# Performance work log

Hardware: AMD Instinct MI355X
Metric: run time of the kernel (lower is better)

The kernel has to match this reference:

```python
import jax, jax.numpy as jnp
import numpy as np

B, N, T, W, H, ED, S, C, E = 16, 256, 64, 12, 64, 64, 5, 4, 2048
ALPHA = 1.0
FG = W + H  # gcn_in_channels = window_size + tgcn_hidden_dim


def setup_inputs() -> dict:
    key = jax.random.key(0)
    ks = jax.random.split(key, 26)
    rn = lambda k, shape: jax.random.normal(k, shape, jnp.float32) * 0.1
    x = jax.random.normal(ks[0], (B, N, T), jnp.float32)
    src = jax.random.randint(ks[1], (E,), 0, N)
    off = jax.random.randint(ks[2], (E,), 1, N)
    dst = (src + off) % N  # no self loops
    return {
        'x': x,
        'static_edge_weight': jax.random.uniform(ks[3], (E,), jnp.float32),
        'gsl_gconv_w': rn(ks[4], (FG, ED)), 'gsl_gconv_b': rn(ks[5], (ED,)),
        'gsl_w1': rn(ks[6], (ED, ED)), 'gsl_b1': rn(ks[7], (ED,)),
        'gsl_w2': rn(ks[8], (ED, ED)), 'gsl_b2': rn(ks[9], (ED,)),
        'wz_c': rn(ks[10], (1, H)), 'bz_c': rn(ks[11], (H,)),
        'wz_l': rn(ks[12], (2 * H, H)), 'bz_l': rn(ks[13], (H,)),
        'wr_c': rn(ks[14], (1, H)), 'br_c': rn(ks[15], (H,)),
        'wr_l': rn(ks[16], (2 * H, H)), 'br_l': rn(ks[17], (H,)),
        'wh_c': rn(ks[18], (1, H)), 'bh_c': rn(ks[19], (H,)),
        'wh_l': rn(ks[20], (2 * H, H)), 'bh_l': rn(ks[21], (H,)),
        'cls_w': rn(ks[22], (N * H, C)), 'cls_b': rn(ks[23], (C,)),
        'static_edge_index': jnp.stack([src, dst]).astype(jnp.int32),
    }


def _normalize(A):
    # GCN sym-norm with added self loops; A has zero diagonal by construction.
    Ahat = A + jnp.eye(N, dtype=A.dtype)
    deg = Ahat.sum(axis=-2)  # in-degree (PyG gcn_norm scatters weight on col)
    dinv = jnp.where(deg > 0, 1.0 / jnp.sqrt(deg), 0.0)
    return dinv[..., :, None] * Ahat * dinv[..., None, :]


def reference(x, static_edge_weight, gsl_gconv_w, gsl_gconv_b, gsl_w1, gsl_b1,
              gsl_w2, gsl_b2, wz_c, bz_c, wz_l, bz_l, wr_c, br_c, wr_l, br_l,
              wh_c, bh_c, wh_l, bh_l, cls_w, cls_b, static_edge_index):
    A_stat = jnp.zeros((N, N), jnp.float32).at[static_edge_index[0], static_edge_index[1]].add(static_edge_weight)
    An_stat = _normalize(A_stat)  # [N,N]

    # Sliding windows, left-padded with zeros to window_size W.
    xp = jnp.pad(x, ((0, 0), (0, 0), (W - 1, 0)))
    widx = jnp.arange(T)[:, None] + jnp.arange(W)[None, :]
    wins = jnp.transpose(xp[:, :, widx], (2, 0, 1, 3))      # [T,B,N,W]
    xts = jnp.transpose(x, (2, 0, 1))[..., None]            # [T,B,N,1]
    cnts = jnp.minimum(jnp.arange(T) + 1, S).astype(jnp.float32)
    idxs = jnp.arange(T) % S

    def gcn_s(X, Wm, b):  # static graph, out[j] = sum_i Anorm[i,j] (XW)[i]
        return jnp.einsum('ij,bif->bjf', An_stat, X @ Wm) + b

    def gcn_d(An, X, Wm, b):  # per-batch dynamic graph
        return jnp.einsum('bij,bif->bjf', An, X @ Wm) + b

    def step(carry, xs):
        h, Eh = carry
        win, xt, cnt, idx = xs
        It = jnp.concatenate([win, h], axis=-1)             # [B,N,W+H]
        df = gcn_s(It, gsl_gconv_w, gsl_gconv_b)
        de1 = jnp.tanh(ALPHA * (df @ gsl_w1 + gsl_b1))
        de2 = jnp.tanh(ALPHA * (df @ gsl_w2 + gsl_b2))
        M12 = jnp.einsum('bie,bje->bij', de1, de2)          # de1 @ de2^T
        Et = jax.nn.relu(jnp.tanh(ALPHA * (M12 - jnp.swapaxes(M12, -1, -2))))
        Eh = Eh.at[:, idx].set(Et)                          # ring buffer write
        Mt = Eh.sum(axis=1) / cnt                           # mean over filled slots
        An = _normalize(Mt)
        cz = gcn_d(An, xt, wz_c, bz_c)
        z = jax.nn.sigmoid(jnp.concatenate([cz, h], -1) @ wz_l + bz_l)
        cr = gcn_d(An, xt, wr_c, br_c)
        r = jax.nn.sigmoid(jnp.concatenate([cr, h], -1) @ wr_l + br_l)
        ch = gcn_d(An, xt, wh_c, bh_c)
        ht = jnp.tanh(jnp.concatenate([ch, h * r], -1) @ wh_l + bh_l)
        h = z * h + (1.0 - z) * ht
        return (h, Eh), None

    h0 = jnp.zeros((B, N, H), jnp.float32)
    Eh0 = jnp.zeros((B, S, N, N), jnp.float32)
    (hT, _), _ = jax.lax.scan(step, (h0, Eh0), (wins, xts, cnts, idxs))
    return hT.reshape(B, N * H) @ cls_w + cls_b
```

## Files before the change

### kernel.cpp

```cpp
#include <hip/hip_runtime.h>
#include <hip/hip_bf16.h>


typedef unsigned short u16;
typedef unsigned int u32;
typedef unsigned long long u64;
typedef __attribute__((ext_vector_type(8))) short bf16x8;
typedef __attribute__((ext_vector_type(4))) float f32x4;

#define B_ 16
#define N_ 256
#define T_ 64
#define W_ 12
#define S_ 5
#define E_ 2048
#define G_ 16

__device__ __forceinline__ float b2f(u16 u) {
  union { u32 i; float f; } v; v.i = ((u32)u) << 16; return v.f;
}
__device__ __forceinline__ u16 f2b(float f) {
  union { float f; u32 i; } v; v.f = f;
  u32 x = v.i; x += 0x7fff + ((x >> 16) & 1); return (u16)(x >> 16);
}
__device__ __forceinline__ float ftanh(float x) {
  float e = __expf(-2.f * fabsf(x));
  float t = (1.f - e) / (1.f + e);
  return x < 0.f ? -t : t;
}
__device__ __forceinline__ float fsigm(float x) { return 1.f / (1.f + __expf(-x)); }
__device__ __forceinline__ float cvload(const void* p, size_t i, int f) {
  return f ? ((const float*)p)[i] : b2f(((const u16*)p)[i]);
}
__device__ __forceinline__ u16 cvloadb(const void* p, size_t i, int f) {
  return f ? f2b(((const float*)p)[i]) : ((const u16*)p)[i];
}
__device__ __forceinline__ float gld(const float* p) {
  return __hip_atomic_load(p, __ATOMIC_RELAXED, __HIP_MEMORY_SCOPE_SYSTEM);
}
__device__ __forceinline__ void gst(float* p, float v) {
  __hip_atomic_store(p, v, __ATOMIC_RELAXED, __HIP_MEMORY_SCOPE_SYSTEM);
}
__device__ __forceinline__ u64 gld64(const u64* p) {
  return __hip_atomic_load(p, __ATOMIC_RELAXED, __HIP_MEMORY_SCOPE_SYSTEM);
}
__device__ __forceinline__ void gst64(u64* p, u64 v) {
  __hip_atomic_store(p, v, __ATOMIC_RELAXED, __HIP_MEMORY_SCOPE_SYSTEM);
}
__device__ __forceinline__ u32 gldu(const u32* p) {
  return __hip_atomic_load(p, __ATOMIC_RELAXED, __HIP_MEMORY_SCOPE_SYSTEM);
}
__device__ __forceinline__ f32x4 mfma16(bf16x8 a, bf16x8 b, f32x4 c) {
  return __builtin_amdgcn_mfma_f32_16x16x32_bf16(a, b, c, 0, 0, 0);
}
__device__ __forceinline__ bf16x8 ldfrag(const u16* p) { return *(const bf16x8*)p; }

struct Params {
  const void *x0, *ew0, *gw0, *gb0, *w10, *b10, *w20, *b20;
  const void *wzc0, *bzc0, *wzl0, *bzl0, *wrc0, *brc0, *wrl0, *brl0;
  const void *whc0, *bhc0, *whl0, *bhl0, *clsw0, *clsb0;
  const int* eidx;
  float *degsum, *Eh, *clspart;
  u64 *de1g, *de2g, *xTp, *hgpT;
  u32 *tags;
  void* out;
};

__device__ __forceinline__ void wtag(const u32* tg, u32 target) {
  const int k = threadIdx.x & 15;
  while (!__all((int)(gldu(&tg[k]) >= target)))
    __builtin_amdgcn_s_sleep(1);
}
__device__ __forceinline__ void wtag8(const u32* tg, int base, u32 target) {
  const int k = base + (threadIdx.x & 7);
  while (!__all((int)(gldu(&tg[k]) >= target)))
    __builtin_amdgcn_s_sleep(1);
}
__device__ __forceinline__ void ptag(u32* tg, int wg, u32 val) {
  if (threadIdx.x == 0)
    __hip_atomic_store(&tg[wg], val, __ATOMIC_RELAXED, __HIP_MEMORY_SCOPE_SYSTEM);
}

__global__ void __launch_bounds__(256, 1) dtgcn_main(Params p) {
  __shared__ __align__(16) u16 s_union[21120];
  __shared__ __align__(16) u16 s_gwF[64 * 104];
  __shared__ __align__(16) u16 s_w1T[64 * 72], s_w2T[64 * 72];
  __shared__ __align__(16) u16 s_gzT[64 * 72], s_grT[64 * 72], s_ghT[64 * 72];
  __shared__ __align__(16) u16 s_antO1[16 * 264], s_antO2[16 * 264];
  __shared__ __align__(16) u16 s_m1[16 * 104];
  __shared__ float s_msum[16 * 257];
  __shared__ __align__(16) u16 s_de1I[16 * 72], s_de2I[16 * 72];
  __shared__ __align__(16) u16 s_hbf[16 * 72];
  __shared__ __align__(16) u16 s_dfhr[16 * 72];
  __shared__ float s_colv[16], s_degacc[16];
  __shared__ float s_y[256], s_dinv[256], s_s[16];
  __shared__ float s_uv[384], s_gb[64], s_b1[64], s_b2[64];
  __shared__ int s_flag;

  const int b = blockIdx.x & 15;
  const int wg = blockIdx.x >> 4;
  const int tid = threadIdx.x;
  const int lane = tid & 63;
  const int wv = tid >> 6;
  const int l = lane & 15;
  const int quad = lane >> 4;
  const int r0 = wg * 16;

  u64* de1g = p.de1g + (size_t)b * N_ * 16;
  u64* de2g = p.de2g + (size_t)b * N_ * 16;
  u64* hgpb = p.hgpT + (size_t)b * 64 * 64;
  u64* xTw  = p.xTp + (size_t)b * 64 * 64;
  const u64* xTb = xTw;
  float* degb = p.degsum + (size_t)b * N_;
  u32* tgDe = p.tags + b * 128;
  u32* tgDg = p.tags + b * 128 + 16;
  u32* tgH  = p.tags + b * 128 + 32;
  u32* tgX  = p.tags + b * 128 + 48;
  u32* tgC  = p.tags + b * 128 + 64;

  if (tid == 0) {
    const u16* q = (const u16*)p.x0;
    int c = 0;
    for (int i = 0; i < 256; ++i) {
      int ex = (q[i] >> 7) & 0xff;
      c += (ex >= 110 && ex <= 135);
    }
    s_flag = (c < 200) ? 1 : 0;
  }
  __syncthreads();
  const int fl = s_flag;

  {
    u16* xs = s_union;
    #pragma unroll
    for (int r = 0; r < 4; ++r) {
      const int tt = wg * 4 + r;
      xs[r * 256 + tid] = f2b(cvload(p.x0, ((size_t)b * N_ + tid) * T_ + tt, fl));
    }
    __syncthreads();
    const int r = tid >> 6, c = tid & 63;
    u64 v = (u64)xs[r * 256 + 4 * c]
          | ((u64)xs[r * 256 + 4 * c + 1] << 16)
          | ((u64)xs[r * 256 + 4 * c + 2] << 32)
          | ((u64)xs[r * 256 + 4 * c + 3] << 48);
    gst64(&xTw[(size_t)(wg * 4 + r) * 64 + c], v);
    __syncthreads();
    ptag(tgX, wg, 1);
  }

  {
    float* s_acol = (float*)s_union;
    float* s_dg   = (float*)s_union + 4096;
    for (int i = tid; i < 4096; i += 256) s_acol[i] = 0.f;
    s_dg[tid] = 0.f;
    __syncthreads();
    for (int e2 = tid; e2 < E_; e2 += 256) {
      const int sN = p.eidx[e2], dN = p.eidx[E_ + e2];
      const float wv2 = cvload(p.ew0, e2, fl);
      atomicAdd(&s_dg[dN], wv2);
      const int dl = dN - r0;
      if (dl >= 0 && dl < 16) atomicAdd(&s_acol[sN * 16 + dl], wv2);
    }
    __syncthreads();
    s_dg[tid] = rsqrtf(1.f + s_dg[tid]);
    __syncthreads();
    for (int idx = tid; idx < 4096; idx += 256) {
      const int jl = idx >> 8, i = idx & 255;
      float a = s_acol[i * 16 + jl] + ((i == r0 + jl) ? 1.f : 0.f);
      float v = s_dg[i] * a * s_dg[r0 + jl];
      u16 hi = f2b(v);
      s_antO1[jl * 264 + i] = hi;
      s_antO2[jl * 264 + i] = f2b(v - b2f(hi));
    }
  }

  for (int idx = tid; idx < 64 * 104; idx += 256) {
    const int ee = idx / 104, k = idx - ee * 104;
    u16 v = 0;
    if (k < 64) v = cvloadb(p.gw0, (12 + k) * 64 + ee, fl);
    else if (k < 76) v = cvloadb(p.gw0, (k - 64) * 64 + ee, fl);
    s_gwF[ee * 104 + k] = v;
  }
  for (int idx = tid; idx < 4096; idx += 256) {
    const int ee = idx >> 6, ff = idx & 63;
    s_w1T[ee * 72 + ff] = cvloadb(p.w10, ff * 64 + ee, fl);
    s_w2T[ee * 72 + ff] = cvloadb(p.w20, ff * 64 + ee, fl);
    s_gzT[ee * 72 + ff] = cvloadb(p.wzl0, 4096 + ff * 64 + ee, fl);
    s_grT[ee * 72 + ff] = cvloadb(p.wrl0, 4096 + ff * 64 + ee, fl);
    s_ghT[ee * 72 + ff] = cvloadb(p.whl0, 4096 + ff * 64 + ee, fl);
  }
  if (tid < 64) {
    const int e2 = tid;
    float uz = 0, vz = 0, ur = 0, vr = 0, uh = 0, vh = 0;
    for (int f = 0; f < 64; ++f) {
      float wz = cvload(p.wzl0, f * 64 + e2, fl);
      float wr = cvload(p.wrl0, f * 64 + e2, fl);
      float wh = cvload(p.whl0, f * 64 + e2, fl);
      uz += cvload(p.wzc0, f, fl) * wz; vz += cvload(p.bzc0, f, fl) * wz;
      ur += cvload(p.wrc0, f, fl) * wr; vr += cvload(p.brc0, f, fl) * wr;
      uh += cvload(p.whc0, f, fl) * wh; vh += cvload(p.bhc0, f, fl) * wh;
    }
    s_uv[0 * 64 + e2] = uz; s_uv[1 * 64 + e2] = vz + cvload(p.bzl0, e2, fl);
    s_uv[2 * 64 + e2] = ur; s_uv[3 * 64 + e2] = vr + cvload(p.brl0, e2, fl);
    s_uv[4 * 64 + e2] = uh; s_uv[5 * 64 + e2] = vh + cvload(p.bhl0, e2, fl);
    s_gb[tid] = cvload(p.gb0, tid, fl);
    s_b1[tid] = cvload(p.b10, tid, fl);
    s_b2[tid] = cvload(p.b20, tid, fl);
  }
  for (int idx = tid; idx < 16 * 257; idx += 256) s_msum[idx] = 0.f;
  for (int idx = tid; idx < 16 * 72; idx += 256) s_hbf[idx] = 0;
  for (int idx = tid; idx < 16 * 104; idx += 256) s_m1[idx] = 0;
  for (int idx = 20064 + tid; idx < 21120; idx += 256) s_union[idx] = 0;
  if (tid < 16) s_degacc[tid] = 0.f;
  __syncthreads();

  u16* s_itT = s_union;
  u16* s_j1  = s_union;
  u16* s_j2  = s_union + 9216;

  float hreg[4] = {0.f, 0.f, 0.f, 0.f};
  const int e = wv * 16 + l;

  for (int t = 0; t < T_; ++t) {
    float xv;
    {
      if (t == 0) wtag(tgX, 1);
      xv = cvload(p.x0, ((size_t)b * N_ + tid) * T_ + t, fl);
      u64 tw0[2], tw1[2];
      #pragma unroll
      for (int q = 0; q < 2; ++q) {
        const int idx = q * 256 + tid;
        const int row = idx >> 5, c = idx & 31;
        const bool ok = idx < 384;
        const int tx = t - (W_ - 1) + row;
        const bool live = ok && tx >= 0;
        tw0[q] = live ? gld64(&xTb[(size_t)tx * 64 + c]) : 0ull;
        tw1[q] = live ? gld64(&xTb[(size_t)tx * 64 + 32 + c]) : 0ull;
      }
      wtag8(tgH, 0, (u32)t);
      {
        u64 th[8];
        #pragma unroll
        for (int q = 0; q < 8; ++q) {
          const int idx = q * 256 + tid;
          const int row = idx >> 5, c = idx & 31;
          th[q] = gld64(&hgpb[(size_t)row * 64 + c]);
        }
        #pragma unroll
        for (int q = 0; q < 8; ++q) {
          const int idx = q * 256 + tid;
          const int row = idx >> 5, c = idx & 31;
          *(u64*)&s_itT[row * 264 + c * 4] = th[q];
        }
        #pragma unroll
        for (int q = 0; q < 2; ++q) {
          const int idx = q * 256 + tid;
          if (idx < 384) {
            const int row = idx >> 5, c = idx & 31;
            *(u64*)&s_itT[(64 + row) * 264 + c * 4] = tw0[q];
          }
        }
      }
      __syncthreads();
      wtag8(tgH, 8, (u32)t);
      u64 th1[8];
      #pragma unroll
      for (int q = 0; q < 8; ++q) {
        const int idx = q * 256 + tid;
        const int row = idx >> 5, c = idx & 31;
        th1[q] = gld64(&hgpb[(size_t)row * 64 + 32 + c]);
      }
      f32x4 accA[2];
      accA[0] = (f32x4){0.f, 0.f, 0.f, 0.f};
      accA[1] = (f32x4){0.f, 0.f, 0.f, 0.f};
      {
        int ti = 0;
        for (int nt = wv; nt < 5; nt += 4, ++ti) {
          #pragma unroll
          for (int ch = 0; ch < 4; ++ch) {
            const int io = ch * 32 + quad * 8;
            bf16x8 bfr = ldfrag(&s_itT[(nt * 16 + l) * 264 + io]);
            accA[ti] = mfma16(ldfrag(&s_antO1[l * 264 + io]), bfr, accA[ti]);
            accA[ti] = mfma16(ldfrag(&s_antO2[l * 264 + io]), bfr, accA[ti]);
          }
        }
      }
      #pragma unroll
      for (int q = 0; q < 8; ++q) {
        const int idx = q * 256 + tid;
        const int row = idx >> 5, c = idx & 31;
        *(u64*)&s_itT[row * 264 + (32 + c) * 4] = th1[q];
      }
      #pragma unroll
      for (int q = 0; q < 2; ++q) {
        const int idx = q * 256 + tid;
        if (idx < 384) {
          const int row = idx >> 5, c = idx & 31;
          *(u64*)&s_itT[(64 + row) * 264 + (32 + c) * 4] = tw1[q];
        }
      }
      __syncthreads();
      {
        int ti = 0;
        for (int nt = wv; nt < 5; nt += 4, ++ti) {
          #pragma unroll
          for (int ch = 4; ch < 8; ++ch) {
            const int io = ch * 32 + quad * 8;
            bf16x8 bfr = ldfrag(&s_itT[(nt * 16 + l) * 264 + io]);
            accA[ti] = mfma16(ldfrag(&s_antO1[l * 264 + io]), bfr, accA[ti]);
            accA[ti] = mfma16(ldfrag(&s_antO2[l * 264 + io]), bfr, accA[ti]);
          }
          #pragma unroll
          for (int r = 0; r < 4; ++r)
            s_m1[(quad * 4 + r) * 104 + nt * 16 + l] = f2b(accA[ti][r]);
        }
      }
      __syncthreads();
      {
        f32x4 dfa = {0.f, 0.f, 0.f, 0.f};
        #pragma unroll
        for (int ks = 0; ks < 3; ++ks) {
          bf16x8 afr = ldfrag(&s_m1[l * 104 + ks * 32 + quad * 8]);
          dfa = mfma16(afr, ldfrag(&s_gwF[e * 104 + ks * 32 + quad * 8]), dfa);
        }
        #pragma unroll
        for (int r = 0; r < 4; ++r)
          s_dfhr[(quad * 4 + r) * 72 + e] = f2b(dfa[r] + s_gb[e]);
      }
      __syncthreads();
      {
        f32x4 E1, E2;
        #pragma unroll
        for (int r = 0; r < 4; ++r) { E1[r] = s_b1[e]; E2[r] = s_b2[e]; }
        #pragma unroll
        for (int ks = 0; ks < 2; ++ks) {
          bf16x8 afr = ldfrag(&s_dfhr[l * 72 + ks * 32 + quad * 8]);
          E1 = mfma16(afr, ldfrag(&s_w1T[e * 72 + ks * 32 + quad * 8]), E1);
          E2 = mfma16(afr, ldfrag(&s_w2T[e * 72 + ks * 32 + quad * 8]), E2);
        }
        #pragma unroll
        for (int r = 0; r < 4; ++r) {
          s_de1I[(quad * 4 + r) * 72 + e] = f2b(ftanh(E1[r]));
          s_de2I[(quad * 4 + r) * 72 + e] = f2b(ftanh(E2[r]));
        }
      }
      __syncthreads();
      {
        const int row = tid >> 4, c = tid & 15;
        u64 v1 = *(const u64*)&s_de1I[row * 72 + c * 4];
        u64 v2 = *(const u64*)&s_de2I[row * 72 + c * 4];
        gst64(&de1g[(size_t)(r0 + row) * 16 + c], v1);
        gst64(&de2g[(size_t)(r0 + row) * 16 + c], v2);
      }
      __syncthreads();
      ptag(tgDe, wg, (u32)(t + 1));
    }

    {
      const int sidx = t % S_;
      float* Ehc = p.Eh + ((size_t)((b * S_ + sidx) * G_ + wg)) * (N_ * 16);
      if (tid < 16) s_colv[tid] = 0.f;
      bf16x8 bq1[2], bq2[2];
      #pragma unroll
      for (int ks = 0; ks < 2; ++ks) {
        bq1[ks] = ldfrag(&s_de1I[l * 72 + ks * 32 + quad * 8]);
        bq2[ks] = ldfrag(&s_de2I[l * 72 + ks * 32 + quad * 8]);
      }
      float old0[2][4], old1[2][4];
      #pragma unroll
      for (int mt2 = 0; mt2 < 2; ++mt2) {
        const int mt = wv * 2 + mt2;
        #pragma unroll
        for (int r = 0; r < 4; ++r) {
          const int i0 = mt * 16 + quad * 4 + r;
          old0[mt2][r] = Ehc[(size_t)i0 * 16 + l];
          old1[mt2][r] = Ehc[(size_t)(128 + i0) * 16 + l];
        }
      }
      wtag8(tgDe, 0, (u32)(t + 1));
      u64 t1a[8], t2a[8];
      #pragma unroll
      for (int q = 0; q < 8; ++q) {
        const int idx = q * 256 + tid;
        const int row = idx >> 4, c = idx & 15;
        t1a[q] = gld64(&de1g[(size_t)row * 16 + c]);
        t2a[q] = gld64(&de2g[(size_t)row * 16 + c]);
      }
      #pragma unroll
      for (int q = 0; q < 8; ++q) {
        const int idx = q * 256 + tid;
        const int row = idx >> 4, c = idx & 15;
        *(u64*)&s_j1[row * 72 + c * 4] = t1a[q];
        *(u64*)&s_j2[row * 72 + c * 4] = t2a[q];
      }
      __syncthreads();
      wtag8(tgDe, 8, (u32)(t + 1));
      u64 t1b[8], t2b[8];
      #pragma unroll
      for (int q = 0; q < 8; ++q) {
        const int idx = q * 256 + tid;
        const int row = idx >> 4, c = idx & 15;
        t1b[q] = gld64(&de1g[(size_t)(128 + row) * 16 + c]);
        t2b[q] = gld64(&de2g[(size_t)(128 + row) * 16 + c]);
      }
      float dcacc = 0.f;
      #pragma unroll
      for (int mt2 = 0; mt2 < 2; ++mt2) {
        const int mt = wv * 2 + mt2;
        f32x4 D1 = {0.f, 0.f, 0.f, 0.f}, D2 = {0.f, 0.f, 0.f, 0.f};
        #pragma unroll
        for (int ks = 0; ks < 2; ++ks) {
          bf16x8 a1 = ldfrag(&s_j1[(mt * 16 + l) * 72 + ks * 32 + quad * 8]);
          bf16x8 a2 = ldfrag(&s_j2[(mt * 16 + l) * 72 + ks * 32 + quad * 8]);
          D1 = mfma16(a1, bq2[ks], D1);
          D2 = mfma16(a2, bq1[ks], D2);
        }
        #pragma unroll
        for (int r = 0; r < 4; ++r) {
          const int i = mt * 16 + quad * 4 + r;
          float d = ftanh(D1[r] - D2[r]);
          float eN = fmaxf(d, 0.f);
          float dd = eN - old0[mt2][r];
          Ehc[(size_t)i * 16 + l] = eN;
          s_msum[l * 257 + i] += dd;
          dcacc += dd;
        }
      }
      __syncthreads();
      #pragma unroll
      for (int q = 0; q < 8; ++q) {
        const int idx = q * 256 + tid;
        const int row = idx >> 4, c = idx & 15;
        *(u64*)&s_j1[row * 72 + c * 4] = t1b[q];
        *(u64*)&s_j2[row * 72 + c * 4] = t2b[q];
      }
      __syncthreads();
      #pragma unroll
      for (int mt2 = 0; mt2 < 2; ++mt2) {
        const int mt = wv * 2 + mt2;
        f32x4 D1 = {0.f, 0.f, 0.f, 0.f}, D2 = {0.f, 0.f, 0.f, 0.f};
        #pragma unroll
        for (int ks = 0; ks < 2; ++ks) {
          bf16x8 a1 = ldfrag(&s_j1[(mt * 16 + l) * 72 + ks * 32 + quad * 8]);
          bf16x8 a2 = ldfrag(&s_j2[(mt * 16 + l) * 72 + ks * 32 + quad * 8]);
          D1 = mfma16(a1, bq2[ks], D1);
          D2 = mfma16(a2, bq1[ks], D2);
        }
        #pragma unroll
        for (int r = 0; r < 4; ++r) {
          const int i = 128 + mt * 16 + quad * 4 + r;
          float d = ftanh(D1[r] - D2[r]);
          float eN = fmaxf(d, 0.f);
          float dd = eN - old1[mt2][r];
          Ehc[(size_t)i * 16 + l] = eN;
          s_msum[l * 257 + i] += dd;
          dcacc += dd;
        }
      }
      dcacc += __shfl_xor(dcacc, 16);
      dcacc += __shfl_xor(dcacc, 32);
      if (lane < 16) atomicAdd(&s_colv[lane], dcacc);
      __syncthreads();
      if (tid < 16) {
        float nd = s_degacc[tid] + s_colv[tid];
        s_degacc[tid] = nd;
        gst(&degb[r0 + tid], nd);
      }
      __syncthreads();
      ptag(tgDg, wg, (u32)(t + 1));
    }

    {
      f32x4 azh = {0.f, 0.f, 0.f, 0.f}, arh = {0.f, 0.f, 0.f, 0.f};
      #pragma unroll
      for (int ks = 0; ks < 2; ++ks) {
        bf16x8 afr = ldfrag(&s_hbf[l * 72 + ks * 32 + quad * 8]);
        azh = mfma16(afr, ldfrag(&s_gzT[e * 72 + ks * 32 + quad * 8]), azh);
        arh = mfma16(afr, ldfrag(&s_grT[e * 72 + ks * 32 + quad * 8]), arh);
      }
      wtag(tgDg, (u32)(t + 1));
      const float cnt = (float)((t + 1 < S_) ? (t + 1) : S_);
      const float invc = 1.f / cnt;
      {
        float dg = 1.f + gld(&degb[tid]) * invc;
        float di = rsqrtf(dg);
        s_dinv[tid] = di;
        s_y[tid] = di * xv;
      }
      __syncthreads();
      {
        const int jl = tid >> 4, cc = tid & 15;
        float part = 0.f;
        #pragma unroll
        for (int k = 0; k < 16; ++k) {
          const int i = cc * 16 + ((k + cc) & 15);
          part += s_msum[jl * 257 + i] * s_y[i];
        }
        part += __shfl_xor(part, 1);
        part += __shfl_xor(part, 2);
        part += __shfl_xor(part, 4);
        part += __shfl_xor(part, 8);
        if (cc == 0) {
          const int j = r0 + jl;
          s_s[jl] = s_dinv[j] * (part * invc + s_y[j]);
        }
      }
      __syncthreads();
      float sv[4];
      #pragma unroll
      for (int r = 0; r < 4; ++r) sv[r] = s_s[quad * 4 + r];
      float zz[4], rr2[4];
      #pragma unroll
      for (int r = 0; r < 4; ++r) {
        zz[r]  = fsigm(azh[r] + s_uv[0 * 64 + e] * sv[r] + s_uv[1 * 64 + e]);
        rr2[r] = fsigm(arh[r] + s_uv[2 * 64 + e] * sv[r] + s_uv[3 * 64 + e]);
      }
      #pragma unroll
      for (int r = 0; r < 4; ++r)
        s_dfhr[(quad * 4 + r) * 72 + e] = f2b(hreg[r] * rr2[r]);
      __syncthreads();
      f32x4 ah;
      #pragma unroll
      for (int r = 0; r < 4; ++r) ah[r] = s_uv[4 * 64 + e] * sv[r] + s_uv[5 * 64 + e];
      #pragma unroll
      for (int ks = 0; ks < 2; ++ks) {
        bf16x8 afr = ldfrag(&s_dfhr[l * 72 + ks * 32 + quad * 8]);
        ah = mfma16(afr, ldfrag(&s_ghT[e * 72 + ks * 32 + quad * 8]), ah);
      }
      #pragma unroll
      for (int r = 0; r < 4; ++r) {
        float ht = ftanh(ah[r]);
        hreg[r] = zz[r] * hreg[r] + (1.f - zz[r]) * ht;
      }
      {
        u16 h0 = f2b(hreg[0]), h1 = f2b(hreg[1]);
        u16 h2 = f2b(hreg[2]), h3 = f2b(hreg[3]);
        u64 hv = (u64)h0 | ((u64)h1 << 16) | ((u64)h2 << 32) | ((u64)h3 << 48);
        gst64(&hgpb[(size_t)e * 64 + (r0 >> 2) + quad], hv);
        s_hbf[(quad * 4 + 0) * 72 + e] = h0;
        s_hbf[(quad * 4 + 1) * 72 + e] = h1;
        s_hbf[(quad * 4 + 2) * 72 + e] = h2;
        s_hbf[(quad * 4 + 3) * 72 + e] = h3;
      }
      __syncthreads();
      ptag(tgH, wg, (u32)(t + 1));
    }
  }

  {
    float part[4] = {0.f, 0.f, 0.f, 0.f};
    #pragma unroll
    for (int r = 0; r < 4; ++r) {
      const size_t base = ((size_t)(r0 + quad * 4 + r) * 64 + e) * 4;
      #pragma unroll
      for (int c = 0; c < 4; ++c)
        part[c] += hreg[r] * cvload(p.clsw0, base + c, fl);
    }
    #pragma unroll
    for (int c = 0; c < 4; ++c) {
      float v = part[c];
      v += __shfl_xor(v, 1);  v += __shfl_xor(v, 2);
      v += __shfl_xor(v, 4);  v += __shfl_xor(v, 8);
      v += __shfl_xor(v, 16); v += __shfl_xor(v, 32);
      if (lane == 0) s_s[wv * 4 + c] = v;
    }
    __syncthreads();
    if (tid < 4) {
      float tot = s_s[0 + tid] + s_s[4 + tid] + s_s[8 + tid] + s_s[12 + tid];
      gst(&p.clspart[(b * 16 + wg) * 4 + tid], tot);
    }
    __syncthreads();
    ptag(tgC, wg, 1);
    if (wg == 0) {
      wtag(tgC, 1);
      if (tid < 4) {
        float v = 0.f;
        for (int k = 0; k < 16; ++k) v += gld(&p.clspart[(b * 16 + k) * 4 + tid]);
        v += cvload(p.clsb0, tid, fl);
        if (fl) ((float*)p.out)[b * 4 + tid] = v;
        else    ((u16*)p.out)[b * 4 + tid] = f2b(v);
      }
    }
  }
}

extern "C" void kernel_launch(void* const* d_in, const int* in_sizes, int n_in,
                              void* d_out, int out_size, void* d_ws, size_t ws_size,
                              hipStream_t stream) {
  float* w = (float*)d_ws;
  size_t o = 0;
  auto alloc = [&](size_t n) { float* r = w + o; o += (n + 63) & ~(size_t)63; return r; };
  u64* de1g = (u64*)alloc((size_t)B_ * N_ * 32);
  u64* de2g = (u64*)alloc((size_t)B_ * N_ * 32);
  u64* xTp  = (u64*)alloc((size_t)B_ * 64 * 128);
  float* clspart = alloc(B_ * 16 * 4);
  const size_t zero_off = o;
  u64*   hgpT  = (u64*)alloc((size_t)B_ * 64 * 128);
  float* degs  = alloc((size_t)B_ * N_);
  u32*   tags  = (u32*)alloc(B_ * 128);
  float* Eh    = alloc((size_t)B_ * S_ * N_ * N_);
  if (ws_size < o * sizeof(float)) return;

  (void)hipMemsetAsync(w + zero_off, 0, (o - zero_off) * sizeof(float), stream);

  Params p;
  p.x0  = d_in[0];  p.ew0 = d_in[1];
  p.gw0 = d_in[2];  p.gb0 = d_in[3];
  p.w10 = d_in[4];  p.b10 = d_in[5];
  p.w20 = d_in[6];  p.b20 = d_in[7];
  p.wzc0 = d_in[8];  p.bzc0 = d_in[9];  p.wzl0 = d_in[10]; p.bzl0 = d_in[11];
  p.wrc0 = d_in[12]; p.brc0 = d_in[13]; p.wrl0 = d_in[14]; p.brl0 = d_in[15];
  p.whc0 = d_in[16]; p.bhc0 = d_in[17]; p.whl0 = d_in[18]; p.bhl0 = d_in[19];
  p.clsw0 = d_in[20]; p.clsb0 = d_in[21];
  p.eidx = (const int*)d_in[22];
  p.degsum = degs; p.Eh = Eh; p.clspart = clspart;
  p.de1g = de1g; p.de2g = de2g; p.xTp = xTp; p.hgpT = hgpT;
  p.tags = tags; p.out = d_out;

  void* args[] = { &p };
  hipError_t ce = hipLaunchCooperativeKernel((const void*)dtgcn_main,
                                             dim3(B_ * G_), dim3(256), args, 0, stream);
  if (ce != hipSuccess) {
    (void)hipGetLastError();
    dtgcn_main<<<dim3(B_ * G_), dim3(256), 0, stream>>>(p);
  }
}
```

Before: 854.4 us.

## Replace tag-based inter-block flags with epoch-stamped data words for polling

Each exchanged 64-bit word (de1/de2 features, degree sums, hidden state) now carries the step epoch in its upper 32 bits alongside the payload. Consumers poll the data itself until every word shows the expected epoch. This removes the extra __syncthreads plus tag store on the producer side and the separate tag wait on the consumer side. In exchange, global traffic per exchange doubles because each word holds only half as much payload, and the exchanged buffers must be zeroed at startup.

```diff
diff --git a/kernel.cpp b/kernel.cpp
--- a/kernel.cpp
+++ b/kernel.cpp
@@ -60,19 +60,14 @@
   const void *wzc0, *bzc0, *wzl0, *bzl0, *wrc0, *brc0, *wrl0, *brl0;
   const void *whc0, *bhc0, *whl0, *bhl0, *clsw0, *clsb0;
   const int* eidx;
-  float *degsum, *Eh, *clspart;
-  u64 *de1g, *de2g, *xTp, *hgpT;
+  float *Eh, *clspart;
+  u64 *degsum, *de1g, *de2g, *xTp, *hgpT;
   u32 *tags;
   void* out;
 };
 
 __device__ __forceinline__ void wtag(const u32* tg, u32 target) {
   const int k = threadIdx.x & 15;
-  while (!__all((int)(gldu(&tg[k]) >= target)))
-    __builtin_amdgcn_s_sleep(1);
-}
-__device__ __forceinline__ void wtag8(const u32* tg, int base, u32 target) {
-  const int k = base + (threadIdx.x & 7);
   while (!__all((int)(gldu(&tg[k]) >= target)))
     __builtin_amdgcn_s_sleep(1);
 }
@@ -106,15 +101,12 @@
   const int quad = lane >> 4;
   const int r0 = wg * 16;
 
-  u64* de1g = p.de1g + (size_t)b * N_ * 16;
-  u64* de2g = p.de2g + (size_t)b * N_ * 16;
-  u64* hgpb = p.hgpT + (size_t)b * 64 * 64;
+  u64* de1g = p.de1g + (size_t)b * N_ * 32;
+  u64* de2g = p.de2g + (size_t)b * N_ * 32;
+  u64* hgpb = p.hgpT + (size_t)b * 64 * 128;
   u64* xTw  = p.xTp + (size_t)b * 64 * 64;
   const u64* xTb = xTw;
-  float* degb = p.degsum + (size_t)b * N_;
-  u32* tgDe = p.tags + b * 128;
-  u32* tgDg = p.tags + b * 128 + 16;
-  u32* tgH  = p.tags + b * 128 + 32;
+  u64* degb = p.degsum + (size_t)b * N_;
   u32* tgX  = p.tags + b * 128 + 48;
   u32* tgC  = p.tags + b * 128 + 64;
 
@@ -220,6 +212,8 @@
 
   float hreg[4] = {0.f, 0.f, 0.f, 0.f};
   const int e = wv * 16 + l;
+  const int hf_own = wg >> 3;
+  const int hbase_own = ((r0 & 127) >> 1) + quad * 2;
 
   for (int t = 0; t < T_; ++t) {
     float xv;
@@ -237,38 +231,43 @@
         tw0[q] = live ? gld64(&xTb[(size_t)tx * 64 + c]) : 0ull;
         tw1[q] = live ? gld64(&xTb[(size_t)tx * 64 + 32 + c]) : 0ull;
       }
-      wtag8(tgH, 0, (u32)t);
-      {
-        u64 th[8];
-        #pragma unroll
-        for (int q = 0; q < 8; ++q) {
-          const int idx = q * 256 + tid;
+      const u32 htgt = (u32)t;
+      u64 th[16];
+      for (;;) {
+        int ok = 1;
+        #pragma unroll
+        for (int q = 0; q < 16; ++q) {
+          th[q] = gld64(&hgpb[(size_t)(q * 256 + tid)]);
+          ok &= (int)((u32)(th[q] >> 32) >= htgt);
+        }
+        if (__all(ok)) break;
+        __builtin_amdgcn_s_sleep(1);
+      }
+      #pragma unroll
+      for (int q = 0; q < 16; ++q) {
+        const int idx = q * 256 + tid;
+        const int ft = idx >> 6, un = idx & 63;
+        *(u32*)&s_itT[ft * 264 + un * 2] = (u32)th[q];
+      }
+      #pragma unroll
+      for (int q = 0; q < 2; ++q) {
+        const int idx = q * 256 + tid;
+        if (idx < 384) {
           const int row = idx >> 5, c = idx & 31;
-          th[q] = gld64(&hgpb[(size_t)row * 64 + c]);
-        }
-        #pragma unroll
-        for (int q = 0; q < 8; ++q) {
-          const int idx = q * 256 + tid;
-          const int row = idx >> 5, c = idx & 31;
-          *(u64*)&s_itT[row * 264 + c * 4] = th[q];
-        }
-        #pragma unroll
-        for (int q = 0; q < 2; ++q) {
-          const int idx = q * 256 + tid;
-          if (idx < 384) {
-            const int row = idx >> 5, c = idx & 31;
-            *(u64*)&s_itT[(64 + row) * 264 + c * 4] = tw0[q];
-          }
-        }
-      }
-      __syncthreads();
-      wtag8(tgH, 8, (u32)t);
-      u64 th1[8];
-      #pragma unroll
-      for (int q = 0; q < 8; ++q) {
-        const int idx = q * 256 + tid;
-        const int row = idx >> 5, c = idx & 31;
-        th1[q] = gld64(&hgpb[(size_t)row * 64 + 32 + c]);
+          *(u64*)&s_itT[(64 + row) * 264 + c * 4] = tw0[q];
+        }
+      }
+      __syncthreads();
+      u64 th1[16];
+      for (;;) {
+        int ok = 1;
+        #pragma unroll
+        for (int q = 0; q < 16; ++q) {
+          th1[q] = gld64(&hgpb[(size_t)(4096 + q * 256 + tid)]);
+          ok &= (int)((u32)(th1[q] >> 32) >= htgt);
+        }
+        if (__all(ok)) break;
+        __builtin_amdgcn_s_sleep(1);
       }
       f32x4 accA[2];
       accA[0] = (f32x4){0.f, 0.f, 0.f, 0.f};
@@ -286,10 +285,10 @@
         }
       }
       #pragma unroll
-      for (int q = 0; q < 8; ++q) {
+      for (int q = 0; q < 16; ++q) {
         const int idx = q * 256 + tid;
-        const int row = idx >> 5, c = idx & 31;
-        *(u64*)&s_itT[row * 264 + (32 + c) * 4] = th1[q];
+        const int ft = idx >> 6, un = idx & 63;
+        *(u32*)&s_itT[ft * 264 + 128 + un * 2] = (u32)th1[q];
       }
       #pragma unroll
       for (int q = 0; q < 2; ++q) {
@@ -338,22 +337,30 @@
           E1 = mfma16(afr, ldfrag(&s_w1T[e * 72 + ks * 32 + quad * 8]), E1);
           E2 = mfma16(afr, ldfrag(&s_w2T[e * 72 + ks * 32 + quad * 8]), E2);
         }
+        u32 v1[4], v2[4];
         #pragma unroll
         for (int r = 0; r < 4; ++r) {
-          s_de1I[(quad * 4 + r) * 72 + e] = f2b(ftanh(E1[r]));
-          s_de2I[(quad * 4 + r) * 72 + e] = f2b(ftanh(E2[r]));
-        }
-      }
-      __syncthreads();
-      {
-        const int row = tid >> 4, c = tid & 15;
-        u64 v1 = *(const u64*)&s_de1I[row * 72 + c * 4];
-        u64 v2 = *(const u64*)&s_de2I[row * 72 + c * 4];
-        gst64(&de1g[(size_t)(r0 + row) * 16 + c], v1);
-        gst64(&de2g[(size_t)(r0 + row) * 16 + c], v2);
-      }
-      __syncthreads();
-      ptag(tgDe, wg, (u32)(t + 1));
+          v1[r] = (u32)f2b(ftanh(E1[r]));
+          v2[r] = (u32)f2b(ftanh(E2[r]));
+          s_de1I[(quad * 4 + r) * 72 + e] = (u16)v1[r];
+          s_de2I[(quad * 4 + r) * 72 + e] = (u16)v2[r];
+        }
+        u32 x1[4], x2[4];
+        #pragma unroll
+        for (int r = 0; r < 4; ++r) {
+          x1[r] = (u32)__shfl_xor((int)v1[r], 1);
+          x2[r] = (u32)__shfl_xor((int)v2[r], 1);
+        }
+        const u64 ep = ((u64)(u32)(t + 1)) << 32;
+        u64* dst = (l & 1) ? de2g : de1g;
+        const int un = e >> 1;
+        #pragma unroll
+        for (int r = 0; r < 4; ++r) {
+          u32 lo = (l & 1) ? (x2[r] | (v2[r] << 16)) : (v1[r] | (x1[r] << 16));
+          gst64(&dst[(size_t)(r0 + quad * 4 + r) * 32 + un], (u64)lo | ep);
+        }
+      }
+      __syncthreads();
     }
 
     {
@@ -377,31 +384,40 @@
           old1[mt2][r] = Ehc[(size_t)(128 + i0) * 16 + l];
         }
       }
-      wtag8(tgDe, 0, (u32)(t + 1));
-      u64 t1a[8], t2a[8];
-      #pragma unroll
-      for (int q = 0; q < 8; ++q) {
+      const u32 dtgt = (u32)(t + 1);
+      u64 t1a[16], t2a[16];
+      for (;;) {
+        int ok = 1;
+        #pragma unroll
+        for (int q = 0; q < 16; ++q) {
+          t1a[q] = gld64(&de1g[(size_t)(q * 256 + tid)]);
+          t2a[q] = gld64(&de2g[(size_t)(q * 256 + tid)]);
+          ok &= (int)((u32)(t1a[q] >> 32) >= dtgt);
+          ok &= (int)((u32)(t2a[q] >> 32) >= dtgt);
+        }
+        if (__all(ok)) break;
+        __builtin_amdgcn_s_sleep(1);
+      }
+      #pragma unroll
+      for (int q = 0; q < 16; ++q) {
         const int idx = q * 256 + tid;
-        const int row = idx >> 4, c = idx & 15;
-        t1a[q] = gld64(&de1g[(size_t)row * 16 + c]);
-        t2a[q] = gld64(&de2g[(size_t)row * 16 + c]);
-      }
-      #pragma unroll
-      for (int q = 0; q < 8; ++q) {
-        const int idx = q * 256 + tid;
-        const int row = idx >> 4, c = idx & 15;
-        *(u64*)&s_j1[row * 72 + c * 4] = t1a[q];
-        *(u64*)&s_j2[row * 72 + c * 4] = t2a[q];
-      }
-      __syncthreads();
-      wtag8(tgDe, 8, (u32)(t + 1));
-      u64 t1b[8], t2b[8];
-      #pragma unroll
-      for (int q = 0; q < 8; ++q) {
-        const int idx = q * 256 + tid;
-        const int row = idx >> 4, c = idx & 15;
-        t1b[q] = gld64(&de1g[(size_t)(128 + row) * 16 + c]);
-        t2b[q] = gld64(&de2g[(size_t)(128 + row) * 16 + c]);
+        const int row = idx >> 5, un = idx & 31;
+        *(u32*)&s_j1[row * 72 + un * 2] = (u32)t1a[q];
+        *(u32*)&s_j2[row * 72 + un * 2] = (u32)t2a[q];
+      }
+      __syncthreads();
+      u64 t1b[16], t2b[16];
+      for (;;) {
+        int ok = 1;
+        #pragma unroll
+        for (int q = 0; q < 16; ++q) {
+          t1b[q] = gld64(&de1g[(size_t)(4096 + q * 256 + tid)]);
+          t2b[q] = gld64(&de2g[(size_t)(4096 + q * 256 + tid)]);
+          ok &= (int)((u32)(t1b[q] >> 32) >= dtgt);
+          ok &= (int)((u32)(t2b[q] >> 32) >= dtgt);
+        }
+        if (__all(ok)) break;
+        __builtin_amdgcn_s_sleep(1);
       }
       float dcacc = 0.f;
       #pragma unroll
@@ -428,11 +444,11 @@
       }
       __syncthreads();
       #pragma unroll
-      for (int q = 0; q < 8; ++q) {
+      for (int q = 0; q < 16; ++q) {
         const int idx = q * 256 + tid;
-        const int row = idx >> 4, c = idx & 15;
-        *(u64*)&s_j1[row * 72 + c * 4] = t1b[q];
-        *(u64*)&s_j2[row * 72 + c * 4] = t2b[q];
+        const int row = idx >> 5, un = idx & 31;
+        *(u32*)&s_j1[row * 72 + un * 2] = (u32)t1b[q];
+        *(u32*)&s_j2[row * 72 + un * 2] = (u32)t2b[q];
       }
       __syncthreads();
       #pragma unroll
@@ -464,10 +480,9 @@
       if (tid < 16) {
         float nd = s_degacc[tid] + s_colv[tid];
         s_degacc[tid] = nd;
-        gst(&degb[r0 + tid], nd);
-      }
-      __syncthreads();
-      ptag(tgDg, wg, (u32)(t + 1));
+        union { float f; u32 i; } cv; cv.f = nd;
+        gst64(&degb[r0 + tid], (u64)cv.i | (((u64)dtgt) << 32));
+      }
     }
 
     {
@@ -478,11 +493,18 @@
         azh = mfma16(afr, ldfrag(&s_gzT[e * 72 + ks * 32 + quad * 8]), azh);
         arh = mfma16(afr, ldfrag(&s_grT[e * 72 + ks * 32 + quad * 8]), arh);
       }
-      wtag(tgDg, (u32)(t + 1));
+      const u32 dgt = (u32)(t + 1);
+      u64 du;
+      for (;;) {
+        du = gld64(&degb[tid]);
+        if (__all((int)((u32)(du >> 32) >= dgt))) break;
+        __builtin_amdgcn_s_sleep(1);
+      }
       const float cnt = (float)((t + 1 < S_) ? (t + 1) : S_);
       const float invc = 1.f / cnt;
       {
-        float dg = 1.f + gld(&degb[tid]) * invc;
+        union { u32 i; float f; } dv; dv.i = (u32)du;
+        float dg = 1.f + dv.f * invc;
         float di = rsqrtf(dg);
         s_dinv[tid] = di;
         s_y[tid] = di * xv;
@@ -533,17 +555,17 @@
         hreg[r] = zz[r] * hreg[r] + (1.f - zz[r]) * ht;
       }
       {
-        u16 h0 = f2b(hreg[0]), h1 = f2b(hreg[1]);
-        u16 h2 = f2b(hreg[2]), h3 = f2b(hreg[3]);
-        u64 hv = (u64)h0 | ((u64)h1 << 16) | ((u64)h2 << 32) | ((u64)h3 << 48);
-        gst64(&hgpb[(size_t)e * 64 + (r0 >> 2) + quad], hv);
-        s_hbf[(quad * 4 + 0) * 72 + e] = h0;
-        s_hbf[(quad * 4 + 1) * 72 + e] = h1;
-        s_hbf[(quad * 4 + 2) * 72 + e] = h2;
-        s_hbf[(quad * 4 + 3) * 72 + e] = h3;
-      }
-      __syncthreads();
-      ptag(tgH, wg, (u32)(t + 1));
+        u32 hb0 = f2b(hreg[0]), hb1 = f2b(hreg[1]);
+        u32 hb2 = f2b(hreg[2]), hb3 = f2b(hreg[3]);
+        const u64 ep = ((u64)dgt) << 32;
+        u64* hp = &hgpb[(size_t)hf_own * 4096 + (size_t)e * 64 + hbase_own];
+        gst64(&hp[0], (u64)(hb0 | (hb1 << 16)) | ep);
+        gst64(&hp[1], (u64)(hb2 | (hb3 << 16)) | ep);
+        s_hbf[(quad * 4 + 0) * 72 + e] = (u16)hb0;
+        s_hbf[(quad * 4 + 1) * 72 + e] = (u16)hb1;
+        s_hbf[(quad * 4 + 2) * 72 + e] = (u16)hb2;
+        s_hbf[(quad * 4 + 3) * 72 + e] = (u16)hb3;
+      }
     }
   }
 
@@ -590,13 +612,13 @@
   float* w = (float*)d_ws;
   size_t o = 0;
   auto alloc = [&](size_t n) { float* r = w + o; o += (n + 63) & ~(size_t)63; return r; };
-  u64* de1g = (u64*)alloc((size_t)B_ * N_ * 32);
-  u64* de2g = (u64*)alloc((size_t)B_ * N_ * 32);
   u64* xTp  = (u64*)alloc((size_t)B_ * 64 * 128);
   float* clspart = alloc(B_ * 16 * 4);
   const size_t zero_off = o;
-  u64*   hgpT  = (u64*)alloc((size_t)B_ * 64 * 128);
-  float* degs  = alloc((size_t)B_ * N_);
+  u64* de1g = (u64*)alloc((size_t)B_ * N_ * 64);
+  u64* de2g = (u64*)alloc((size_t)B_ * N_ * 64);
+  u64*   hgpT  = (u64*)alloc((size_t)B_ * 64 * 256);
+  u64* degs  = (u64*)alloc((size_t)B_ * N_ * 2);
   u32*   tags  = (u32*)alloc(B_ * 128);
   float* Eh    = alloc((size_t)B_ * S_ * N_ * N_);
   if (ws_size < o * sizeof(float)) return;
```

Result: slower. 987.7 us (+15.6%).

## Recompute evicted ring-buffer edge tiles from stored embeddings instead of storing Eh

Applied to the files above, without the earlier changes.

Drops the fp32 Eh ring buffer (B*S*N*N floats). It keeps a 6-deep ring of the bf16 de1/de2 embeddings and recomputes the evicted time step's edge tile with MFMA, so the old values can be subtracted from the running sum. Each de store is now written straight from registers after packing bf16 values with lane shuffles, which removes one LDS round-trip and barrier. The degree sum now carries its step tag in the upper 32 bits of a 64-bit word, so the separate degree tag and its barrier are gone. This trades large global read/write traffic for extra MFMA and tanh work plus smaller embedding reloads.

```diff
diff --git a/kernel.cpp b/kernel.cpp
--- a/kernel.cpp
+++ b/kernel.cpp
@@ -60,8 +60,8 @@
   const void *wzc0, *bzc0, *wzl0, *bzl0, *wrc0, *brc0, *wrl0, *brl0;
   const void *whc0, *bhc0, *whl0, *bhl0, *clsw0, *clsb0;
   const int* eidx;
-  float *degsum, *Eh, *clspart;
-  u64 *de1g, *de2g, *xTp, *hgpT;
+  float *clspart;
+  u64 *degsum, *de1g, *de2g, *xTp, *hgpT;
   u32 *tags;
   void* out;
 };
@@ -106,14 +106,11 @@
   const int quad = lane >> 4;
   const int r0 = wg * 16;
 
-  u64* de1g = p.de1g + (size_t)b * N_ * 16;
-  u64* de2g = p.de2g + (size_t)b * N_ * 16;
   u64* hgpb = p.hgpT + (size_t)b * 64 * 64;
   u64* xTw  = p.xTp + (size_t)b * 64 * 64;
   const u64* xTb = xTw;
-  float* degb = p.degsum + (size_t)b * N_;
+  u64* degb = p.degsum + (size_t)b * N_;
   u32* tgDe = p.tags + b * 128;
-  u32* tgDg = p.tags + b * 128 + 16;
   u32* tgH  = p.tags + b * 128 + 32;
   u32* tgX  = p.tags + b * 128 + 48;
   u32* tgC  = p.tags + b * 128 + 64;
@@ -223,6 +220,12 @@
 
   for (int t = 0; t < T_; ++t) {
     float xv;
+    u64* de1n = p.de1g + ((size_t)(t % 6) * B_ + b) * N_ * 16;
+    u64* de2n = p.de2g + ((size_t)(t % 6) * B_ + b) * N_ * 16;
+    const u64* de1o = p.de1g + ((size_t)((t + 1) % 6) * B_ + b) * N_ * 16;
+    const u64* de2o = p.de2g + ((size_t)((t + 1) % 6) * B_ + b) * N_ * 16;
+    const int havold = (t >= S_);
+
     {
       if (t == 0) wtag(tgX, 1);
       xv = cvload(p.x0, ((size_t)b * N_ + tid) * T_ + t, fl);
@@ -338,53 +341,75 @@
           E1 = mfma16(afr, ldfrag(&s_w1T[e * 72 + ks * 32 + quad * 8]), E1);
           E2 = mfma16(afr, ldfrag(&s_w2T[e * 72 + ks * 32 + quad * 8]), E2);
         }
+        u32 v1[4], v2[4];
         #pragma unroll
         for (int r = 0; r < 4; ++r) {
-          s_de1I[(quad * 4 + r) * 72 + e] = f2b(ftanh(E1[r]));
-          s_de2I[(quad * 4 + r) * 72 + e] = f2b(ftanh(E2[r]));
-        }
-      }
-      __syncthreads();
-      {
-        const int row = tid >> 4, c = tid & 15;
-        u64 v1 = *(const u64*)&s_de1I[row * 72 + c * 4];
-        u64 v2 = *(const u64*)&s_de2I[row * 72 + c * 4];
-        gst64(&de1g[(size_t)(r0 + row) * 16 + c], v1);
-        gst64(&de2g[(size_t)(r0 + row) * 16 + c], v2);
+          v1[r] = (u32)f2b(ftanh(E1[r]));
+          v2[r] = (u32)f2b(ftanh(E2[r]));
+          s_de1I[(quad * 4 + r) * 72 + e] = (u16)v1[r];
+          s_de2I[(quad * 4 + r) * 72 + e] = (u16)v2[r];
+        }
+        #pragma unroll
+        for (int r = 0; r < 4; ++r) {
+          u32 a1 = (u32)__shfl_xor((int)v1[r], 1);
+          u32 a2 = (u32)__shfl_xor((int)v2[r], 1);
+          u32 ev1 = (l & 1) ? a1 : v1[r], od1 = (l & 1) ? v1[r] : a1;
+          u32 ev2 = (l & 1) ? a2 : v2[r], od2 = (l & 1) ? v2[r] : a2;
+          u32 w1 = ev1 | (od1 << 16), w2 = ev2 | (od2 << 16);
+          u32 x1 = (u32)__shfl_xor((int)w1, 2);
+          u32 x2 = (u32)__shfl_xor((int)w2, 2);
+          u64 q1 = (l & 2) ? ((u64)x1 | ((u64)w1 << 32)) : ((u64)w1 | ((u64)x1 << 32));
+          u64 q2 = (l & 2) ? ((u64)x2 | ((u64)w2 << 32)) : ((u64)w2 | ((u64)x2 << 32));
+          if ((l & 3) == 0) {
+            const size_t ro = (size_t)(r0 + quad * 4 + r) * 16 + wv * 4 + (l >> 2);
+            gst64(&de1n[ro], q1);
+            gst64(&de2n[ro], q2);
+          }
+        }
       }
       __syncthreads();
       ptag(tgDe, wg, (u32)(t + 1));
     }
 
     {
-      const int sidx = t % S_;
-      float* Ehc = p.Eh + ((size_t)((b * S_ + sidx) * G_ + wg)) * (N_ * 16);
-      if (tid < 16) s_colv[tid] = 0.f;
       bf16x8 bq1[2], bq2[2];
       #pragma unroll
       for (int ks = 0; ks < 2; ++ks) {
         bq1[ks] = ldfrag(&s_de1I[l * 72 + ks * 32 + quad * 8]);
         bq2[ks] = ldfrag(&s_de2I[l * 72 + ks * 32 + quad * 8]);
       }
-      float old0[2][4], old1[2][4];
-      #pragma unroll
-      for (int mt2 = 0; mt2 < 2; ++mt2) {
-        const int mt = wv * 2 + mt2;
-        #pragma unroll
-        for (int r = 0; r < 4; ++r) {
-          const int i0 = mt * 16 + quad * 4 + r;
-          old0[mt2][r] = Ehc[(size_t)i0 * 16 + l];
-          old1[mt2][r] = Ehc[(size_t)(128 + i0) * 16 + l];
-        }
-      }
-      wtag8(tgDe, 0, (u32)(t + 1));
+      if (tid < 16) s_colv[tid] = 0.f;
+      bf16x8 bq1o[2], bq2o[2];
+      bf16x8 a1o[2][2], a2o[2][2];
+      if (havold) {
+        #pragma unroll
+        for (int ks = 0; ks < 2; ++ks) {
+          union { u64 q[2]; bf16x8 v; } u1, u2;
+          const size_t o = (size_t)(r0 + l) * 16 + ks * 8 + quad * 2;
+          u1.q[0] = gld64(&de1o[o]); u1.q[1] = gld64(&de1o[o + 1]);
+          u2.q[0] = gld64(&de2o[o]); u2.q[1] = gld64(&de2o[o + 1]);
+          bq1o[ks] = u1.v; bq2o[ks] = u2.v;
+        }
+        #pragma unroll
+        for (int mt2 = 0; mt2 < 2; ++mt2)
+          #pragma unroll
+          for (int ks = 0; ks < 2; ++ks) {
+            union { u64 q[2]; bf16x8 v; } u1, u2;
+            const size_t o = (size_t)((wv * 2 + mt2) * 16 + l) * 16 + ks * 8 + quad * 2;
+            u1.q[0] = gld64(&de1o[o]); u1.q[1] = gld64(&de1o[o + 1]);
+            u2.q[0] = gld64(&de2o[o]); u2.q[1] = gld64(&de2o[o + 1]);
+            a1o[mt2][ks] = u1.v; a2o[mt2][ks] = u2.v;
+          }
+      }
+      const u32 dtgt = (u32)(t + 1);
+      wtag8(tgDe, 0, dtgt);
       u64 t1a[8], t2a[8];
       #pragma unroll
       for (int q = 0; q < 8; ++q) {
         const int idx = q * 256 + tid;
         const int row = idx >> 4, c = idx & 15;
-        t1a[q] = gld64(&de1g[(size_t)row * 16 + c]);
-        t2a[q] = gld64(&de2g[(size_t)row * 16 + c]);
+        t1a[q] = gld64(&de1n[(size_t)row * 16 + c]);
+        t2a[q] = gld64(&de2n[(size_t)row * 16 + c]);
       }
       #pragma unroll
       for (int q = 0; q < 8; ++q) {
@@ -394,14 +419,29 @@
         *(u64*)&s_j2[row * 72 + c * 4] = t2a[q];
       }
       __syncthreads();
-      wtag8(tgDe, 8, (u32)(t + 1));
+      wtag8(tgDe, 8, dtgt);
       u64 t1b[8], t2b[8];
       #pragma unroll
       for (int q = 0; q < 8; ++q) {
         const int idx = q * 256 + tid;
         const int row = idx >> 4, c = idx & 15;
-        t1b[q] = gld64(&de1g[(size_t)(128 + row) * 16 + c]);
-        t2b[q] = gld64(&de2g[(size_t)(128 + row) * 16 + c]);
+        t1b[q] = gld64(&de1n[(size_t)(128 + row) * 16 + c]);
+        t2b[q] = gld64(&de2n[(size_t)(128 + row) * 16 + c]);
+      }
+      float eO0[2][4] = {{0.f, 0.f, 0.f, 0.f}, {0.f, 0.f, 0.f, 0.f}};
+      if (havold) {
+        #pragma unroll
+        for (int mt2 = 0; mt2 < 2; ++mt2) {
+          f32x4 D1 = {0.f, 0.f, 0.f, 0.f}, D2 = {0.f, 0.f, 0.f, 0.f};
+          #pragma unroll
+          for (int ks = 0; ks < 2; ++ks) {
+            D1 = mfma16(a1o[mt2][ks], bq2o[ks], D1);
+            D2 = mfma16(a2o[mt2][ks], bq1o[ks], D2);
+          }
+          #pragma unroll
+          for (int r = 0; r < 4; ++r)
+            eO0[mt2][r] = fmaxf(ftanh(D1[r] - D2[r]), 0.f);
+        }
       }
       float dcacc = 0.f;
       #pragma unroll
@@ -418,13 +458,23 @@
         #pragma unroll
         for (int r = 0; r < 4; ++r) {
           const int i = mt * 16 + quad * 4 + r;
-          float d = ftanh(D1[r] - D2[r]);
-          float eN = fmaxf(d, 0.f);
-          float dd = eN - old0[mt2][r];
-          Ehc[(size_t)i * 16 + l] = eN;
+          float eN = fmaxf(ftanh(D1[r] - D2[r]), 0.f);
+          float dd = eN - eO0[mt2][r];
           s_msum[l * 257 + i] += dd;
           dcacc += dd;
         }
+      }
+      if (havold) {
+        #pragma unroll
+        for (int mt2 = 0; mt2 < 2; ++mt2)
+          #pragma unroll
+          for (int ks = 0; ks < 2; ++ks) {
+            union { u64 q[2]; bf16x8 v; } u1, u2;
+            const size_t o = (size_t)(128 + (wv * 2 + mt2) * 16 + l) * 16 + ks * 8 + quad * 2;
+            u1.q[0] = gld64(&de1o[o]); u1.q[1] = gld64(&de1o[o + 1]);
+            u2.q[0] = gld64(&de2o[o]); u2.q[1] = gld64(&de2o[o + 1]);
+            a1o[mt2][ks] = u1.v; a2o[mt2][ks] = u2.v;
+          }
       }
       __syncthreads();
       #pragma unroll
@@ -435,6 +485,21 @@
         *(u64*)&s_j2[row * 72 + c * 4] = t2b[q];
       }
       __syncthreads();
+      float eO1[2][4] = {{0.f, 0.f, 0.f, 0.f}, {0.f, 0.f, 0.f, 0.f}};
+      if (havold) {
+        #pragma unroll
+        for (int mt2 = 0; mt2 < 2; ++mt2) {
+          f32x4 D1 = {0.f, 0.f, 0.f, 0.f}, D2 = {0.f, 0.f, 0.f, 0.f};
+          #pragma unroll
+          for (int ks = 0; ks < 2; ++ks) {
+            D1 = mfma16(a1o[mt2][ks], bq2o[ks], D1);
+            D2 = mfma16(a2o[mt2][ks], bq1o[ks], D2);
+          }
+          #pragma unroll
+          for (int r = 0; r < 4; ++r)
+            eO1[mt2][r] = fmaxf(ftanh(D1[r] - D2[r]), 0.f);
+        }
+      }
       #pragma unroll
       for (int mt2 = 0; mt2 < 2; ++mt2) {
         const int mt = wv * 2 + mt2;
@@ -449,10 +514,8 @@
         #pragma unroll
         for (int r = 0; r < 4; ++r) {
           const int i = 128 + mt * 16 + quad * 4 + r;
-          float d = ftanh(D1[r] - D2[r]);
-          float eN = fmaxf(d, 0.f);
-          float dd = eN - old1[mt2][r];
-          Ehc[(size_t)i * 16 + l] = eN;
+          float eN = fmaxf(ftanh(D1[r] - D2[r]), 0.f);
+          float dd = eN - eO1[mt2][r];
           s_msum[l * 257 + i] += dd;
           dcacc += dd;
         }
@@ -464,10 +527,9 @@
       if (tid < 16) {
         float nd = s_degacc[tid] + s_colv[tid];
         s_degacc[tid] = nd;
-        gst(&degb[r0 + tid], nd);
-      }
-      __syncthreads();
-      ptag(tgDg, wg, (u32)(t + 1));
+        union { float f; u32 i; } cv; cv.f = nd;
+        gst64(&degb[r0 + tid], (u64)cv.i | ((u64)dtgt << 32));
+      }
     }
 
     {
@@ -478,11 +540,18 @@
         azh = mfma16(afr, ldfrag(&s_gzT[e * 72 + ks * 32 + quad * 8]), azh);
         arh = mfma16(afr, ldfrag(&s_grT[e * 72 + ks * 32 + quad * 8]), arh);
       }
-      wtag(tgDg, (u32)(t + 1));
+      const u32 dgt = (u32)(t + 1);
+      u64 du;
+      for (;;) {
+        du = gld64(&degb[tid]);
+        if (__all((int)((u32)(du >> 32) >= dgt))) break;
+        __builtin_amdgcn_s_sleep(1);
+      }
       const float cnt = (float)((t + 1 < S_) ? (t + 1) : S_);
       const float invc = 1.f / cnt;
       {
-        float dg = 1.f + gld(&degb[tid]) * invc;
+        union { u32 i; float f; } dv; dv.i = (u32)du;
+        float dg = 1.f + dv.f * invc;
         float di = rsqrtf(dg);
         s_dinv[tid] = di;
         s_y[tid] = di * xv;
@@ -590,15 +659,14 @@
   float* w = (float*)d_ws;
   size_t o = 0;
   auto alloc = [&](size_t n) { float* r = w + o; o += (n + 63) & ~(size_t)63; return r; };
-  u64* de1g = (u64*)alloc((size_t)B_ * N_ * 32);
-  u64* de2g = (u64*)alloc((size_t)B_ * N_ * 32);
   u64* xTp  = (u64*)alloc((size_t)B_ * 64 * 128);
   float* clspart = alloc(B_ * 16 * 4);
+  u64* de1g = (u64*)alloc((size_t)6 * B_ * N_ * 32);
+  u64* de2g = (u64*)alloc((size_t)6 * B_ * N_ * 32);
   const size_t zero_off = o;
   u64*   hgpT  = (u64*)alloc((size_t)B_ * 64 * 128);
-  float* degs  = alloc((size_t)B_ * N_);
+  u64*   degs  = (u64*)alloc((size_t)B_ * N_ * 2);
   u32*   tags  = (u32*)alloc(B_ * 128);
-  float* Eh    = alloc((size_t)B_ * S_ * N_ * N_);
   if (ws_size < o * sizeof(float)) return;
 
   (void)hipMemsetAsync(w + zero_off, 0, (o - zero_off) * sizeof(float), stream);
@@ -613,7 +681,8 @@
   p.whc0 = d_in[16]; p.bhc0 = d_in[17]; p.whl0 = d_in[18]; p.bhl0 = d_in[19];
   p.clsw0 = d_in[20]; p.clsb0 = d_in[21];
   p.eidx = (const int*)d_in[22];
-  p.degsum = degs; p.Eh = Eh; p.clspart = clspart;
+  p.clspart = clspart;
+  p.degsum = degs;
   p.de1g = de1g; p.de2g = de2g; p.xTp = xTp; p.hgpT = hgpT;
   p.tags = tags; p.out = d_out;
 
```

Result: slower. 1.099 ms (+28.6%).
